# Optimization experiments

Measured on AMD Instinct MI355X. Metric: run time of the kernel, lower is better.

Reference implementation:

```python
import jax, jax.numpy as jnp
import numpy as np

T, E, H, I, K = 2048, 16, 2048, 1408, 4
NORM_TOPK_PROB = True
W_SCALE = 0.02  # realistic init scale to keep activations sane


def setup_inputs() -> dict:
    key = jax.random.key(0)
    k_x, k_r, k_g, k_u, k_d = jax.random.split(key, 5)
    return {
        "x": jax.random.normal(k_x, (T, H), jnp.float32),
        "router_logits": jax.random.normal(k_r, (T, E), jnp.float32),
        "gate_w": jax.random.normal(k_g, (E, I, H), jnp.float32) * W_SCALE,
        "up_w": jax.random.normal(k_u, (E, I, H), jnp.float32) * W_SCALE,
        "down_w": jax.random.normal(k_d, (E, H, I), jnp.float32) * W_SCALE,
    }


def reference(x, router_logits, gate_w, up_w, down_w):
    # Router: softmax over experts, take top-k, optionally renormalize.
    probs = jax.nn.softmax(router_logits.astype(jnp.float32), axis=-1)  # [T, E]
    top_vals, top_idx = jax.lax.top_k(probs, K)                          # [T, K]
    if NORM_TOPK_PROB:
        top_vals = top_vals / jnp.sum(top_vals, axis=-1, keepdims=True)
    # Dense combine weights [T, E]: zero for unselected experts.
    combine = jnp.einsum("tke,tk->te", jax.nn.one_hot(top_idx, E, dtype=top_vals.dtype), top_vals)
    combine = combine.astype(x.dtype)

    # GLU per expert: down( silu(gate(x)) * up(x) ), combined by routing weights.
    g = jnp.einsum("th,eih->tei", x, gate_w)   # [T, E, I]
    u = jnp.einsum("th,eih->tei", x, up_w)     # [T, E, I]
    h = jax.nn.silu(g) * u                      # [T, E, I]
    out = jnp.einsum("tei,ehi,te->th", h, down_w, combine)  # [T, H]
    return out
```

## Files before the change

### kernel.cpp

```cpp
#include <hip/hip_runtime.h>
#include <math.h>

#define TTOK 2048
#define NEXP 16
#define HDIM 2048
#define IDIM 1408
#define TOPK 4

typedef __attribute__((ext_vector_type(8))) short short8;
typedef __attribute__((ext_vector_type(4))) float floatx4;

#define GUP ((size_t)NEXP * IDIM * HDIM)

#define LDSP(p) ((__attribute__((address_space(3))) void*)(p))
#define GLBP(p) ((const __attribute__((address_space(1))) void*)(p))

__device__ __forceinline__ unsigned short f2bf(float f) {
    unsigned u = __builtin_bit_cast(unsigned, f);
    u += 0x7FFFu + ((u >> 16) & 1u);
    return (unsigned short)(u >> 16);
}

__device__ __forceinline__ void cvt8(const float* __restrict__ s, unsigned short* __restrict__ d) {
    const float4* sv = (const float4*)s;
    float4 a = sv[0], b = sv[1];
    union { unsigned short h[8]; uint4 v; } p;
    p.h[0] = f2bf(a.x); p.h[1] = f2bf(a.y); p.h[2] = f2bf(a.z); p.h[3] = f2bf(a.w);
    p.h[4] = f2bf(b.x); p.h[5] = f2bf(b.y); p.h[6] = f2bf(b.z); p.h[7] = f2bf(b.w);
    *(uint4*)d = p.v;
}

__global__ void zero_i32(int* __restrict__ p, int n) {
    int i = threadIdx.x;
    if (i < n) p[i] = 0;
}

__global__ void cast_weights(const float* __restrict__ g, const float* __restrict__ u,
                             const float* __restrict__ d,
                             unsigned short* __restrict__ og, unsigned short* __restrict__ ou,
                             unsigned short* __restrict__ od) {
    size_t i = ((size_t)blockIdx.x * blockDim.x + threadIdx.x) * 8;
    size_t stride = (size_t)gridDim.x * blockDim.x * 8;
    for (; i < GUP; i += stride) {
        cvt8(g + i, og + i);
        cvt8(u + i, ou + i);
        cvt8(d + i, od + i);
    }
}

__global__ void router_kernel(const float* __restrict__ logits,
                              int* __restrict__ cnt,
                              int* __restrict__ tok_id,
                              float* __restrict__ tok_w,
                              int* __restrict__ tk_ep) {
    int t = blockIdx.x * blockDim.x + threadIdx.x;
    if (t >= TTOK) return;
    float l[NEXP];
#pragma unroll
    for (int e = 0; e < NEXP; ++e) l[e] = logits[t * NEXP + e];
    int bi[TOPK]; float bv[TOPK];
    unsigned used = 0;
#pragma unroll
    for (int k = 0; k < TOPK; ++k) {
        float best = -1e30f; int b = 0;
#pragma unroll
        for (int e = 0; e < NEXP; ++e) {
            if (!((used >> e) & 1u) && l[e] > best) { best = l[e]; b = e; }
        }
        used |= 1u << b; bi[k] = b; bv[k] = best;
    }
    float m = bv[0], w[TOPK], s = 0.f;
#pragma unroll
    for (int k = 0; k < TOPK; ++k) { w[k] = expf(bv[k] - m); s += w[k]; }
    float inv = 1.f / s;
#pragma unroll
    for (int k = 0; k < TOPK; ++k) {
        int e = bi[k];
        int pos = atomicAdd(&cnt[e], 1);
        tok_id[e * TTOK + pos] = t;
        tok_w[e * TTOK + pos] = w[k] * inv;
        tk_ep[t * TOPK + k] = (e << 16) | pos;
    }
}

__global__ void scan_kernel(const int* __restrict__ cnt, int* __restrict__ offs) {
    if (threadIdx.x == 0 && blockIdx.x == 0) {
        int a = 0;
        for (int e = 0; e < NEXP; ++e) {
            offs[e] = a;
            a += (cnt[e] + 127) & ~127;
        }
        offs[NEXP] = a;
    }
}

__global__ void gather_x(const float* __restrict__ x, const int* __restrict__ cnt,
                         const int* __restrict__ offs, const int* __restrict__ tok_id,
                         unsigned short* __restrict__ xg) {
    int e = blockIdx.y, slot = blockIdx.x;
    int n = cnt[e];
    int padcap = (n + 127) & ~127;
    if (slot >= padcap) return;
    unsigned short* dst = xg + (size_t)(offs[e] + slot) * HDIM;
    int tid = threadIdx.x;
    if (slot < n) {
        const float* src = x + (size_t)tok_id[e * TTOK + slot] * HDIM;
        cvt8(src + tid * 8, dst + tid * 8);
    } else {
        uint4 z = {0u, 0u, 0u, 0u};
        ((uint4*)dst)[tid] = z;
    }
}

__launch_bounds__(256)
__global__ void gateup_mfma(const unsigned short* __restrict__ xg,
                            const unsigned short* __restrict__ gw,
                            const unsigned short* __restrict__ uw,
                            const int* __restrict__ cnt, const int* __restrict__ offs,
                            const float* __restrict__ tok_w,
                            unsigned short* __restrict__ hbuf) {
    const int e = blockIdx.z;
    const int n = cnt[e];
    const int m0 = blockIdx.y * 128;
    if (m0 >= n) return;
    const int i0 = blockIdx.x * 128;
    const int rowbase = offs[e];

    __shared__ __align__(16) unsigned short sA[2][128 * 32];
    __shared__ __align__(16) unsigned short sBg[2][128 * 32];
    __shared__ __align__(16) unsigned short sBu[2][128 * 32];

    const int tid = threadIdx.x;
    const int lane = tid & 63;
    const int wave = tid >> 6;
    const int wm = wave >> 1;
    const int wn = wave & 1;

    const unsigned short* Abase = xg + (size_t)(rowbase + m0) * HDIM;
    const unsigned short* Gbase = gw + (size_t)e * IDIM * HDIM + (size_t)i0 * HDIM;
    const unsigned short* Ubase = uw + (size_t)e * IDIM * HDIM + (size_t)i0 * HDIM;

    floatx4 accg[4][4], accu[4][4];
#pragma unroll
    for (int i = 0; i < 4; ++i)
#pragma unroll
        for (int j = 0; j < 4; ++j) {
            accg[i][j] = (floatx4){0.f, 0.f, 0.f, 0.f};
            accu[i][j] = (floatx4){0.f, 0.f, 0.f, 0.f};
        }

    const int srow = lane >> 2;
    const int scol = (lane & 3) * 8;

    auto stage = [&](int buf, int k0) {
#pragma unroll
        for (int q = 0; q < 2; ++q) {
            const int ch = q * 4 + wave;
            const int r = ch * 16 + srow;
            const size_t go = (size_t)r * HDIM + k0 + scol;
            const int lo = ch * 512 + lane * 8;
            __builtin_amdgcn_global_load_lds(GLBP(Abase + go), LDSP(&sA[buf][lo]), 16, 0, 0);
            __builtin_amdgcn_global_load_lds(GLBP(Gbase + go), LDSP(&sBg[buf][lo]), 16, 0, 0);
            __builtin_amdgcn_global_load_lds(GLBP(Ubase + go), LDSP(&sBu[buf][lo]), 16, 0, 0);
        }
    };

    stage(0, 0);
    __syncthreads();

    const int ko = (lane >> 4) * 8;
    const int mrow = wm * 64 + (lane & 15);
    const int nrow = wn * 64 + (lane & 15);

    int cur = 0;
    for (int k0 = 0; k0 < HDIM; k0 += 32) {
        const int nb = cur ^ 1;
        if (k0 + 32 < HDIM) stage(nb, k0 + 32);

        short8 af[4], bg[4], bu[4];
#pragma unroll
        for (int i = 0; i < 4; ++i)
            af[i] = *(const short8*)&sA[cur][(mrow + i * 16) * 32 + ko];
#pragma unroll
        for (int j = 0; j < 4; ++j) {
            bg[j] = *(const short8*)&sBg[cur][(nrow + j * 16) * 32 + ko];
            bu[j] = *(const short8*)&sBu[cur][(nrow + j * 16) * 32 + ko];
        }
#pragma unroll
        for (int i = 0; i < 4; ++i)
#pragma unroll
            for (int j = 0; j < 4; ++j) {
                accg[i][j] = __builtin_amdgcn_mfma_f32_16x16x32_bf16(af[i], bg[j], accg[i][j], 0, 0, 0);
                accu[i][j] = __builtin_amdgcn_mfma_f32_16x16x32_bf16(af[i], bu[j], accu[i][j], 0, 0, 0);
            }
        __syncthreads();
        cur = nb;
    }

    const int qe = lane >> 4;
    const int cl = lane & 15;
#pragma unroll
    for (int i = 0; i < 4; ++i) {
#pragma unroll
        for (int r = 0; r < 4; ++r) {
            int slot = m0 + wm * 64 + i * 16 + qe * 4 + r;
            if (slot < n) {
                float wgt = tok_w[e * TTOK + slot];
                size_t rowoff = (size_t)(rowbase + slot) * IDIM + i0 + wn * 64 + cl;
#pragma unroll
                for (int j = 0; j < 4; ++j) {
                    float g = accg[i][j][r];
                    float u = accu[i][j][r];
                    float h = (g / (1.f + __expf(-g))) * u * wgt;
                    hbuf[rowoff + j * 16] = f2bf(h);
                }
            }
        }
    }
}

__launch_bounds__(256)
__global__ void down_mfma(const unsigned short* __restrict__ hbuf,
                          const unsigned short* __restrict__ dw,
                          const int* __restrict__ cnt, const int* __restrict__ offs,
                          float* __restrict__ pbuf) {
    const int e = blockIdx.z;
    const int n = cnt[e];
    const int m0 = blockIdx.y * 128;
    if (m0 >= n) return;
    const int h0 = blockIdx.x * 128;
    const int rowbase = offs[e];

    __shared__ __align__(16) unsigned short sA[2][128 * 32];
    __shared__ __align__(16) unsigned short sB[2][128 * 32];

    const int tid = threadIdx.x;
    const int lane = tid & 63;
    const int wave = tid >> 6;
    const int wm = wave >> 1;
    const int wn = wave & 1;

    const unsigned short* Abase = hbuf + (size_t)(rowbase + m0) * IDIM;
    const unsigned short* Bbase = dw + (size_t)e * HDIM * IDIM + (size_t)h0 * IDIM;

    floatx4 acc[4][4];
#pragma unroll
    for (int i = 0; i < 4; ++i)
#pragma unroll
        for (int j = 0; j < 4; ++j) acc[i][j] = (floatx4){0.f, 0.f, 0.f, 0.f};

    const int srow = lane >> 2;
    const int scol = (lane & 3) * 8;

    auto stage = [&](int buf, int k0) {
#pragma unroll
        for (int q = 0; q < 2; ++q) {
            const int ch = q * 4 + wave;
            const int r = ch * 16 + srow;
            const size_t go = (size_t)r * IDIM + k0 + scol;
            const int lo = ch * 512 + lane * 8;
            __builtin_amdgcn_global_load_lds(GLBP(Abase + go), LDSP(&sA[buf][lo]), 16, 0, 0);
            __builtin_amdgcn_global_load_lds(GLBP(Bbase + go), LDSP(&sB[buf][lo]), 16, 0, 0);
        }
    };

    stage(0, 0);
    __syncthreads();

    const int ko = (lane >> 4) * 8;
    const int mrow = wm * 64 + (lane & 15);
    const int nrow = wn * 64 + (lane & 15);

    int cur = 0;
    for (int k0 = 0; k0 < IDIM; k0 += 32) {
        const int nb = cur ^ 1;
        if (k0 + 32 < IDIM) stage(nb, k0 + 32);

        short8 af[4], bf[4];
#pragma unroll
        for (int i = 0; i < 4; ++i)
            af[i] = *(const short8*)&sA[cur][(mrow + i * 16) * 32 + ko];
#pragma unroll
        for (int j = 0; j < 4; ++j)
            bf[j] = *(const short8*)&sB[cur][(nrow + j * 16) * 32 + ko];
#pragma unroll
        for (int i = 0; i < 4; ++i)
#pragma unroll
            for (int j = 0; j < 4; ++j)
                acc[i][j] = __builtin_amdgcn_mfma_f32_16x16x32_bf16(af[i], bf[j], acc[i][j], 0, 0, 0);
        __syncthreads();
        cur = nb;
    }

    const int qe = lane >> 4;
    const int cl = lane & 15;
#pragma unroll
    for (int i = 0; i < 4; ++i) {
#pragma unroll
        for (int r = 0; r < 4; ++r) {
            int slot = m0 + wm * 64 + i * 16 + qe * 4 + r;
            if (slot < n) {
                float* orow = pbuf + (size_t)(rowbase + slot) * HDIM + h0 + wn * 64 + cl;
#pragma unroll
                for (int j = 0; j < 4; ++j) orow[j * 16] = acc[i][j][r];
            }
        }
    }
}

__global__ void reduce_out(const float* __restrict__ pbuf, const int* __restrict__ offs,
                           const int* __restrict__ tk_ep, float* __restrict__ out) {
    const int t = blockIdx.x;
    const int tid = threadIdx.x;
    float4 a0 = {0.f, 0.f, 0.f, 0.f}, a1 = {0.f, 0.f, 0.f, 0.f};
#pragma unroll
    for (int k = 0; k < TOPK; ++k) {
        int v = tk_ep[t * TOPK + k];
        int e = v >> 16, pos = v & 0xffff;
        const float4* src = (const float4*)(pbuf + (size_t)(offs[e] + pos) * HDIM + tid * 8);
        float4 b0 = src[0], b1 = src[1];
        a0.x += b0.x; a0.y += b0.y; a0.z += b0.z; a0.w += b0.w;
        a1.x += b1.x; a1.y += b1.y; a1.z += b1.z; a1.w += b1.w;
    }
    float4* dst = (float4*)(out + (size_t)t * HDIM + tid * 8);
    dst[0] = a0; dst[1] = a1;
}

extern "C" void kernel_launch(void* const* d_in, const int* in_sizes, int n_in,
                              void* d_out, int out_size, void* d_ws, size_t ws_size,
                              hipStream_t stream) {
    const float* x      = (const float*)d_in[0];
    const float* logits = (const float*)d_in[1];
    const float* gate_w = (const float*)d_in[2];
    const float* up_w   = (const float*)d_in[3];
    const float* down_w = (const float*)d_in[4];
    float* out = (float*)d_out;

    char* ws = (char*)d_ws;
    int*   cnt    = (int*)(ws);
    int*   offs   = (int*)(ws + 64);
    int*   tok_id = (int*)(ws + 1024);
    float* tok_w  = (float*)(ws + 1024 + TTOK * NEXP * 4);
    int*   tk_ep  = (int*)(ws + 1024 + 2 * TTOK * NEXP * 4);
    unsigned short* gate_bf = (unsigned short*)(ws + (1u << 20));
    unsigned short* up_bf   = gate_bf + GUP;
    unsigned short* down_bf = up_bf + GUP;
    float* pbuf = (float*)(ws + (1u << 20));
    unsigned short* xg   = (unsigned short*)(ws + (size_t)280 * (1u << 20));
    unsigned short* hbuf = (unsigned short*)(ws + (size_t)321 * (1u << 20));

    zero_i32<<<1, 32, 0, stream>>>(cnt, NEXP);
    cast_weights<<<4096, 256, 0, stream>>>(gate_w, up_w, down_w, gate_bf, up_bf, down_bf);
    router_kernel<<<TTOK / 256, 256, 0, stream>>>(logits, cnt, tok_id, tok_w, tk_ep);
    scan_kernel<<<1, 1, 0, stream>>>(cnt, offs);
    {
        dim3 g(TTOK, NEXP);
        gather_x<<<g, 256, 0, stream>>>(x, cnt, offs, tok_id, xg);
    }
    {
        dim3 g(IDIM / 128, TTOK / 128, NEXP);
        gateup_mfma<<<g, 256, 0, stream>>>(xg, gate_bf, up_bf, cnt, offs, tok_w, hbuf);
    }
    {
        dim3 g(HDIM / 128, TTOK / 128, NEXP);
        down_mfma<<<g, 256, 0, stream>>>(hbuf, down_bf, cnt, offs, pbuf);
    }
    reduce_out<<<TTOK, 256, 0, stream>>>(pbuf, offs, tk_ep, out);
}
```

Before: 978.1 us.

## Triple-buffer LDS pipeline with swizzled layout and fine-grained vmcnt waits

Both grouped GEMM kernels move from double to triple buffering. Loads are issued two K-tiles ahead, and each iteration waits only for the oldest tile using explicit vmcnt waits and raw s_barrier instead of a full __syncthreads. The LDS columns are XOR-swizzled to cut bank conflicts on fragment reads, and s_setprio raises wave priority around the MFMA block. This uses more LDS per block, which may lower occupancy, and relies on hand-counted vmcnt values being correct.

```diff
diff --git a/kernel.cpp b/kernel.cpp
--- a/kernel.cpp
+++ b/kernel.cpp
@@ -112,6 +112,7 @@
     }
 }
 
+
 __launch_bounds__(256)
 __global__ void gateup_mfma(const unsigned short* __restrict__ xg,
                             const unsigned short* __restrict__ gw,
@@ -126,9 +127,9 @@
     const int i0 = blockIdx.x * 128;
     const int rowbase = offs[e];
 
-    __shared__ __align__(16) unsigned short sA[2][128 * 32];
-    __shared__ __align__(16) unsigned short sBg[2][128 * 32];
-    __shared__ __align__(16) unsigned short sBu[2][128 * 32];
+    __shared__ __align__(16) unsigned short sA[3][128 * 32];
+    __shared__ __align__(16) unsigned short sBg[3][128 * 32];
+    __shared__ __align__(16) unsigned short sBu[3][128 * 32];
 
     const int tid = threadIdx.x;
     const int lane = tid & 63;
@@ -150,14 +151,14 @@
         }
 
     const int srow = lane >> 2;
-    const int scol = (lane & 3) * 8;
+    const int scolsw = ((lane & 3) ^ ((lane >> 3) & 3)) * 8;
 
     auto stage = [&](int buf, int k0) {
 #pragma unroll
         for (int q = 0; q < 2; ++q) {
             const int ch = q * 4 + wave;
             const int r = ch * 16 + srow;
-            const size_t go = (size_t)r * HDIM + k0 + scol;
+            const size_t go = (size_t)r * HDIM + k0 + scolsw;
             const int lo = ch * 512 + lane * 8;
             __builtin_amdgcn_global_load_lds(GLBP(Abase + go), LDSP(&sA[buf][lo]), 16, 0, 0);
             __builtin_amdgcn_global_load_lds(GLBP(Gbase + go), LDSP(&sBg[buf][lo]), 16, 0, 0);
@@ -165,27 +166,35 @@
         }
     };
 
+    const int NT = HDIM / 32;
     stage(0, 0);
-    __syncthreads();
-
-    const int ko = (lane >> 4) * 8;
+    stage(1, 32);
+    __builtin_amdgcn_sched_barrier(0);
+    asm volatile("s_waitcnt vmcnt(6)" ::: "memory");
+    __builtin_amdgcn_s_barrier();
+    __builtin_amdgcn_sched_barrier(0);
+
+    const int kphys = ((lane >> 4) ^ ((lane >> 1) & 3)) * 8;
     const int mrow = wm * 64 + (lane & 15);
     const int nrow = wn * 64 + (lane & 15);
 
     int cur = 0;
-    for (int k0 = 0; k0 < HDIM; k0 += 32) {
-        const int nb = cur ^ 1;
-        if (k0 + 32 < HDIM) stage(nb, k0 + 32);
+    for (int t = 0; t < NT; ++t) {
+        if (t + 2 < NT) {
+            int b2 = cur + 2; if (b2 >= 3) b2 -= 3;
+            stage(b2, (t + 2) * 32);
+        }
 
         short8 af[4], bg[4], bu[4];
 #pragma unroll
         for (int i = 0; i < 4; ++i)
-            af[i] = *(const short8*)&sA[cur][(mrow + i * 16) * 32 + ko];
+            af[i] = *(const short8*)&sA[cur][(mrow + i * 16) * 32 + kphys];
 #pragma unroll
         for (int j = 0; j < 4; ++j) {
-            bg[j] = *(const short8*)&sBg[cur][(nrow + j * 16) * 32 + ko];
-            bu[j] = *(const short8*)&sBu[cur][(nrow + j * 16) * 32 + ko];
-        }
+            bg[j] = *(const short8*)&sBg[cur][(nrow + j * 16) * 32 + kphys];
+            bu[j] = *(const short8*)&sBu[cur][(nrow + j * 16) * 32 + kphys];
+        }
+        __builtin_amdgcn_s_setprio(1);
 #pragma unroll
         for (int i = 0; i < 4; ++i)
 #pragma unroll
@@ -193,8 +202,16 @@
                 accg[i][j] = __builtin_amdgcn_mfma_f32_16x16x32_bf16(af[i], bg[j], accg[i][j], 0, 0, 0);
                 accu[i][j] = __builtin_amdgcn_mfma_f32_16x16x32_bf16(af[i], bu[j], accu[i][j], 0, 0, 0);
             }
-        __syncthreads();
-        cur = nb;
+        __builtin_amdgcn_s_setprio(0);
+
+        if (t + 1 < NT) {
+            __builtin_amdgcn_sched_barrier(0);
+            if (t + 2 < NT) asm volatile("s_waitcnt vmcnt(6)" ::: "memory");
+            else            asm volatile("s_waitcnt vmcnt(0)" ::: "memory");
+            __builtin_amdgcn_s_barrier();
+            __builtin_amdgcn_sched_barrier(0);
+        }
+        cur += 1; if (cur >= 3) cur -= 3;
     }
 
     const int qe = lane >> 4;
@@ -231,8 +248,8 @@
     const int h0 = blockIdx.x * 128;
     const int rowbase = offs[e];
 
-    __shared__ __align__(16) unsigned short sA[2][128 * 32];
-    __shared__ __align__(16) unsigned short sB[2][128 * 32];
+    __shared__ __align__(16) unsigned short sA[3][128 * 32];
+    __shared__ __align__(16) unsigned short sB[3][128 * 32];
 
     const int tid = threadIdx.x;
     const int lane = tid & 63;
@@ -250,46 +267,62 @@
         for (int j = 0; j < 4; ++j) acc[i][j] = (floatx4){0.f, 0.f, 0.f, 0.f};
 
     const int srow = lane >> 2;
-    const int scol = (lane & 3) * 8;
+    const int scolsw = ((lane & 3) ^ ((lane >> 3) & 3)) * 8;
 
     auto stage = [&](int buf, int k0) {
 #pragma unroll
         for (int q = 0; q < 2; ++q) {
             const int ch = q * 4 + wave;
             const int r = ch * 16 + srow;
-            const size_t go = (size_t)r * IDIM + k0 + scol;
+            const size_t go = (size_t)r * IDIM + k0 + scolsw;
             const int lo = ch * 512 + lane * 8;
             __builtin_amdgcn_global_load_lds(GLBP(Abase + go), LDSP(&sA[buf][lo]), 16, 0, 0);
             __builtin_amdgcn_global_load_lds(GLBP(Bbase + go), LDSP(&sB[buf][lo]), 16, 0, 0);
         }
     };
 
+    const int NT = IDIM / 32;
     stage(0, 0);
-    __syncthreads();
-
-    const int ko = (lane >> 4) * 8;
+    stage(1, 32);
+    __builtin_amdgcn_sched_barrier(0);
+    asm volatile("s_waitcnt vmcnt(4)" ::: "memory");
+    __builtin_amdgcn_s_barrier();
+    __builtin_amdgcn_sched_barrier(0);
+
+    const int kphys = ((lane >> 4) ^ ((lane >> 1) & 3)) * 8;
     const int mrow = wm * 64 + (lane & 15);
     const int nrow = wn * 64 + (lane & 15);
 
     int cur = 0;
-    for (int k0 = 0; k0 < IDIM; k0 += 32) {
-        const int nb = cur ^ 1;
-        if (k0 + 32 < IDIM) stage(nb, k0 + 32);
+    for (int t = 0; t < NT; ++t) {
+        if (t + 2 < NT) {
+            int b2 = cur + 2; if (b2 >= 3) b2 -= 3;
+            stage(b2, (t + 2) * 32);
+        }
 
         short8 af[4], bf[4];
 #pragma unroll
         for (int i = 0; i < 4; ++i)
-            af[i] = *(const short8*)&sA[cur][(mrow + i * 16) * 32 + ko];
+            af[i] = *(const short8*)&sA[cur][(mrow + i * 16) * 32 + kphys];
 #pragma unroll
         for (int j = 0; j < 4; ++j)
-            bf[j] = *(const short8*)&sB[cur][(nrow + j * 16) * 32 + ko];
+            bf[j] = *(const short8*)&sB[cur][(nrow + j * 16) * 32 + kphys];
+        __builtin_amdgcn_s_setprio(1);
 #pragma unroll
         for (int i = 0; i < 4; ++i)
 #pragma unroll
             for (int j = 0; j < 4; ++j)
                 acc[i][j] = __builtin_amdgcn_mfma_f32_16x16x32_bf16(af[i], bf[j], acc[i][j], 0, 0, 0);
-        __syncthreads();
-        cur = nb;
+        __builtin_amdgcn_s_setprio(0);
+
+        if (t + 1 < NT) {
+            __builtin_amdgcn_sched_barrier(0);
+            if (t + 2 < NT) asm volatile("s_waitcnt vmcnt(4)" ::: "memory");
+            else            asm volatile("s_waitcnt vmcnt(0)" ::: "memory");
+            __builtin_amdgcn_s_barrier();
+            __builtin_amdgcn_sched_barrier(0);
+        }
+        cur += 1; if (cur >= 3) cur -= 3;
     }
 
     const int qe = lane >> 4;
```

Result: slower. 1.012 ms (+3.4%).
